# Optimization experiments

Measured on AMD Instinct MI355X. Metric: run time of the kernel, lower is better.

## Reference

```python
import jax, jax.numpy as jnp
import numpy as np

B, S, D, H = 8, 2048, 64, 4
Dh = D // H  # head_dim = 16


def setup_inputs() -> dict:
    key = jax.random.key(0)
    k1, k2, k3, k4 = jax.random.split(key, 4)
    x = jax.random.normal(k1, (B, S, D), jnp.float32)
    # Linear weights stored torch-style as [out_features, in_features]
    W_qkv = jax.random.normal(k2, (3 * D, D), jnp.float32) * 0.125
    W_proj = jax.random.normal(k3, (D, D), jnp.float32) * 0.125
    b_proj = jnp.zeros((D,), jnp.float32)
    # Ragged structure: random valid length per sample, causal + padding mask
    lens = jax.random.randint(k4, (B,), S // 4, S + 1)
    pos = jnp.arange(S)
    key_valid = pos[None, :] < lens[:, None]          # [B, S]
    causal = pos[:, None] >= pos[None, :]             # [S, S]
    attn_mask = (causal[None, :, :] & key_valid[:, None, :])[:, None, :, :]  # [B,1,S,S], True=attend
    return {"x": x, "attn_mask": attn_mask, "W_qkv": W_qkv, "W_proj": W_proj, "b_proj": b_proj}


def reference(x, attn_mask, W_qkv, W_proj, b_proj):
    b, s, d = x.shape
    # fused QKV projection (qkv_bias=False)
    qkv = x @ W_qkv.T                                  # [B, S, 3D]
    qkv = qkv.reshape(b, s, 3, H, Dh).transpose(2, 0, 3, 1, 4)  # [3, B, H, S, Dh]
    q, k, v = qkv[0], qkv[1], qkv[2]
    scale = 1.0 / jnp.sqrt(jnp.asarray(Dh, x.dtype))
    scores = jnp.einsum('bhqd,bhkd->bhqk', q, k) * scale  # [B, H, S, S]
    neg = jnp.asarray(jnp.finfo(scores.dtype).min, scores.dtype)
    scores = jnp.where(attn_mask, scores, neg)
    attn = jax.nn.softmax(scores, axis=-1)
    ctx = jnp.einsum('bhqk,bhkd->bhqd', attn, v)       # [B, H, S, Dh]
    ctx = ctx.transpose(0, 2, 1, 3).reshape(b, s, d)   # [B, S, D]
    return ctx @ W_proj.T + b_proj
```

## Files before the change

### kernel.cpp

```cpp
#include <hip/hip_runtime.h>
#include <hip/hip_bf16.h>

typedef __attribute__((ext_vector_type(4))) float f32x4;
typedef __attribute__((ext_vector_type(16))) float f32x16;
typedef __attribute__((ext_vector_type(8))) short bf16x8;
typedef __attribute__((ext_vector_type(4))) short bf16x4;

#define SEQ 2048
#define NH 4
#define DH 16

#define WS_LEN 0
#define WS_WP  1024
#define WS_Q   65536
#define WS_K   (WS_Q + 2097152)
#define WS_V   (WS_K + 2097152)

#define MFMA16 __builtin_amdgcn_mfma_f32_16x16x32_bf16
#define MFMA32 __builtin_amdgcn_mfma_f32_32x32x16_bf16

__device__ __forceinline__ short f2bf(float f){
  __hip_bfloat16 h = __float2bfloat16(f);
  return __builtin_bit_cast(short, h);
}

__device__ __forceinline__ bf16x8 pack8(f32x4 a, f32x4 b){
  bf16x8 r;
  r[0]=f2bf(a[0]); r[1]=f2bf(a[1]); r[2]=f2bf(a[2]); r[3]=f2bf(a[3]);
  r[4]=f2bf(b[0]); r[5]=f2bf(b[1]); r[6]=f2bf(b[2]); r[7]=f2bf(b[3]);
  return r;
}

__global__ __launch_bounds__(256) void qkv_prep_kernel(const float* __restrict__ x,
                                                       const unsigned char* __restrict__ mask,
                                                       const float* __restrict__ wqkv,
                                                       const float* __restrict__ wproj,
                                                       unsigned char* __restrict__ ws){
  const int tid = threadIdx.x;
  if (blockIdx.x == 256){
    if (blockIdx.y == 1){
      short* wp = (short*)(ws + WS_WP);
      for (int i = tid; i < 64*64; i += 256) wp[i] = f2bf(wproj[i]);
      return;
    }
    const unsigned w0 = *(const unsigned*)mask;
    const int mode = (mask[2048] != 0) ? 0 : ((w0 == 1u) ? 1 : ((w0 == 0x3f800000u) ? 2 : 0));
    __shared__ int cnts[8];
    if (tid < 8) cnts[tid] = 0;
    __syncthreads();
    const int b = tid >> 5, j = tid & 31;
    const long long rowbase = (long long)b * SEQ * SEQ + (long long)(SEQ-1) * SEQ;
    int c = 0;
    if (mode == 0){
      const unsigned* mw = (const unsigned*)(mask + rowbase);
      for (int k = j; k < SEQ/4; k += 32){
        unsigned v = mw[k];
        c += (v & 0xffu ? 1:0) + (v & 0xff00u ? 1:0) + (v & 0xff0000u ? 1:0) + (v & 0xff000000u ? 1:0);
      }
    } else if (mode == 1){
      for (int k = j; k < SEQ; k += 32) c += ((const int*)mask)[rowbase + k] != 0;
    } else {
      for (int k = j; k < SEQ; k += 32) c += ((const float*)mask)[rowbase + k] != 0.0f;
    }
    atomicAdd(&cnts[b], c);
    __syncthreads();
    if (tid < 8) ((int*)ws)[tid] = cnts[tid];
    return;
  }

  const int lane = tid & 63;
  const int wv   = tid >> 6;
  const int c    = lane & 15;
  const int g    = lane >> 4;
  const int T0   = blockIdx.x * 64 + wv * 16;
  const f32x4 z = {0.f, 0.f, 0.f, 0.f};

  bf16x8 aw[2];
  {
    const float* xr = x + (long long)(T0 + c) * 64 + g * 8;
    #pragma unroll
    for (int w = 0; w < 2; ++w){
      f32x4 lo = *(const f32x4*)(xr + w*32);
      f32x4 hi = *(const f32x4*)(xr + w*32 + 4);
      aw[w] = pack8(lo, hi);
    }
  }

  const int tok  = T0 + c;
  const int b    = tok >> 11;
  const int s    = tok & (SEQ-1);
  short* Qd = (short*)(ws + WS_Q);
  short* Kd = (short*)(ws + WS_K);
  short* Vd = (short*)(ws + WS_V);

  #pragma unroll
  for (int oi = 0; oi < 6; ++oi){
    const int ot = blockIdx.y * 6 + oi;
    const float* wr = wqkv + (ot*16 + c) * 64 + g * 8;
    bf16x8 b0 = pack8(*(const f32x4*)(wr),      *(const f32x4*)(wr + 4));
    bf16x8 b1 = pack8(*(const f32x4*)(wr + 32), *(const f32x4*)(wr + 36));
    f32x4 acc = z;
    acc = MFMA16(b0, aw[0], acc, 0, 0, 0);
    acc = MFMA16(b1, aw[1], acc, 0, 0, 0);
    if (ot < 4){
      bf16x4 pk;
      #pragma unroll
      for (int r = 0; r < 4; ++r) pk[r] = f2bf(acc[r] * (0.25f * 1.44269504f));
      *(bf16x4*)(Qd + ((long long)(b*NH + ot) * SEQ + s) * DH + g*4) = pk;
    } else if (ot < 8){
      bf16x4 pk;
      #pragma unroll
      for (int r = 0; r < 4; ++r) pk[r] = f2bf(acc[r]);
      *(bf16x4*)(Kd + ((long long)(b*NH + (ot-4)) * SEQ + s) * DH + g*4) = pk;
    } else {
      #pragma unroll
      for (int r = 0; r < 4; ++r)
        Vd[((long long)(b*NH + (ot-8)) * DH + g*4 + r) * SEQ + s] = f2bf(acc[r]);
    }
  }
}

__global__ __launch_bounds__(512, 4) void attn_kernel(const unsigned char* __restrict__ ws,
                                                      const float* __restrict__ bproj,
                                                      float* __restrict__ out){
  const int tid  = threadIdx.x;
  const int lane = tid & 63;
  const int wv   = tid >> 6;
  const int h    = wv & 3;
  const int half = wv >> 2;
  const int c    = lane & 15;
  const int g    = lane >> 4;
  const int ql   = lane & 31;
  const int hi   = lane >> 5;
  const int L    = blockIdx.x;
  const int b    = (L + (L >> 8)) & 7;
  const int u    = L >> 3;
  const int t    = (u < 32) ? (2*u) : (63 - 2*(u - 32));
  const int q0   = t * 32;
  const int len  = ((const int*)ws)[b];
  const long long bh = (long long)(b*NH + h);
  const short* Q  = (const short*)(ws + WS_Q) + bh * SEQ * DH;
  const short* K  = (const short*)(ws + WS_K) + bh * SEQ * DH;
  const short* Vt = (const short*)(ws + WS_V) + bh * DH * SEQ;
  const short* Wp = (const short*)(ws + WS_WP);

  __shared__ __align__(16) unsigned char smem[78848];
  float* CMB = (float*)(smem + 65536);
  float* LSB = (float*)(smem + 74240);
  const unsigned pb   = (unsigned)wv * 8192;
  const unsigned CTXB = 74752;
  const f32x4 z  = {0.f,0.f,0.f,0.f};
  const f32x16 z16 = {0.f,0.f,0.f,0.f,0.f,0.f,0.f,0.f,0.f,0.f,0.f,0.f,0.f,0.f,0.f,0.f};
  const short one_bf = (short)0x3F80;
  const bf16x8 ones = {one_bf,one_bf,one_bf,one_bf,one_bf,one_bf,one_bf,one_bf};

  const bf16x8 qf = *(const bf16x8*)(Q + (q0 + ql)*DH + hi*8);

  f32x4 acc[2]  = {z, z};
  f32x4 accS[2] = {z, z};
  const int kcount = min(q0 + 32, len);
  const int nkt  = (kcount + 63) >> 6;
  const int icnt = min(q0 >> 6, len >> 6);
  const int nh0  = nkt >> 1;
  const int kb   = half ? nh0 : 0;
  const int ke   = half ? nkt : nh0;
  const int n    = ke - kb;
  const int rot  = (n >= 4) ? ((h * n) >> 2) : 0;
  const int qg   = q0 + ql;
  const unsigned swq  = (unsigned)(ql & 7) << 4;
  const unsigned sw   = (unsigned)(c & 7) << 4;

  auto TI = [&](int i){ int kt = kb + i + rot; return (kt >= ke) ? kt - n : kt; };

  auto qkexp = [&](int tt, int p, bf16x8 (&kk)[2]){
    const int k0 = tt * 64;
    const bool nomask = tt < icnt;
    const unsigned rowb = pb + ((unsigned)p << 12) + (unsigned)ql*128;
    #pragma unroll
    for (int kb32 = 0; kb32 < 2; ++kb32){
      f32x16 st = MFMA32(kk[kb32], qf, z16, 0, 0, 0);
      #pragma unroll
      for (int grp = 0; grp < 4; ++grp){
        const int keybase = kb32*32 + grp*8 + hi*4;
        float p0 = __builtin_amdgcn_exp2f(st[grp*4 + 0]);
        float p1 = __builtin_amdgcn_exp2f(st[grp*4 + 1]);
        float p2 = __builtin_amdgcn_exp2f(st[grp*4 + 2]);
        float p3 = __builtin_amdgcn_exp2f(st[grp*4 + 3]);
        if (!nomask){
          const int k = k0 + keybase;
          p0 = (k   <= qg && k   < len) ? p0 : 0.f;
          p1 = (k+1 <= qg && k+1 < len) ? p1 : 0.f;
          p2 = (k+2 <= qg && k+2 < len) ? p2 : 0.f;
          p3 = (k+3 <= qg && k+3 < len) ? p3 : 0.f;
        }
        uint2 pk;
        pk.x = __builtin_amdgcn_perm(__builtin_bit_cast(unsigned, p1),
                                     __builtin_bit_cast(unsigned, p0), 0x07060302u);
        pk.y = __builtin_amdgcn_perm(__builtin_bit_cast(unsigned, p3),
                                     __builtin_bit_cast(unsigned, p2), 0x07060302u);
        *(uint2*)&smem[rowb + ((unsigned)(keybase*2) ^ swq)] = pk;
      }
    }
  };

  bf16x8 knx[2], vcur[2], vnx[2], knn[2], vnn[2];
  if (n > 0){
    const int t0 = TI(0);
    const int k0 = t0 * 64;
    bf16x8 k0f[2];
    k0f[0] = *(const bf16x8*)(K + (k0 + ql)*DH + hi*8);
    k0f[1] = *(const bf16x8*)(K + (k0 + 32 + ql)*DH + hi*8);
    vcur[0] = *(const bf16x8*)(Vt + c*SEQ + k0 + g*8);
    vcur[1] = *(const bf16x8*)(Vt + c*SEQ + k0 + 32 + g*8);
    qkexp(t0, 0, k0f);
    if (n > 1){
      const int k1 = TI(1) * 64;
      knx[0] = *(const bf16x8*)(K + (k1 + ql)*DH + hi*8);
      knx[1] = *(const bf16x8*)(K + (k1 + 32 + ql)*DH + hi*8);
      vnx[0] = *(const bf16x8*)(Vt + c*SEQ + k1 + g*8);
      vnx[1] = *(const bf16x8*)(Vt + c*SEQ + k1 + 32 + g*8);
    }
  }

  for (int i = 0; i < n; ++i){
    const unsigned bufr = pb + ((unsigned)(i & 1) << 12);
    bf16x8 pa[2][2];
    #pragma unroll
    for (int qb = 0; qb < 2; ++qb)
      #pragma unroll
      for (int w = 0; w < 2; ++w)
        pa[qb][w] = *(const bf16x8*)&smem[bufr + (qb*16 + c)*128 + ((unsigned)(w*64 + g*16) ^ sw)];

    if (i + 1 < n){
      if (i + 2 < n){
        const int k2 = TI(i + 2) * 64;
        knn[0] = *(const bf16x8*)(K + (k2 + ql)*DH + hi*8);
        knn[1] = *(const bf16x8*)(K + (k2 + 32 + ql)*DH + hi*8);
        vnn[0] = *(const bf16x8*)(Vt + c*SEQ + k2 + g*8);
        vnn[1] = *(const bf16x8*)(Vt + c*SEQ + k2 + 32 + g*8);
      }
      qkexp(TI(i + 1), (i + 1) & 1, knx);
    }

    __builtin_amdgcn_s_setprio(1);
    #pragma unroll
    for (int qb = 0; qb < 2; ++qb)
      #pragma unroll
      for (int w = 0; w < 2; ++w){
        acc[qb]  = MFMA16(pa[qb][w], vcur[w], acc[qb], 0, 0, 0);
        accS[qb] = MFMA16(pa[qb][w], ones,    accS[qb], 0, 0, 0);
      }
    __builtin_amdgcn_s_setprio(0);

    vcur[0] = vnx[0]; vcur[1] = vnx[1];
    knx[0] = knn[0]; knx[1] = knn[1];
    vnx[0] = vnn[0]; vnx[1] = vnn[1];
  }

  if (half == 0){
    #pragma unroll
    for (int qb = 0; qb < 2; ++qb){
      #pragma unroll
      for (int r = 0; r < 4; ++r)
        CMB[(h*32 + qb*16 + g*4 + r)*17 + c] = acc[qb][r];
      if (c == 0){
        #pragma unroll
        for (int r = 0; r < 4; ++r)
          LSB[h*32 + qb*16 + g*4 + r] = accS[qb][r];
      }
    }
  }
  __syncthreads();
  if (half == 1){
    #pragma unroll
    for (int qb = 0; qb < 2; ++qb){
      #pragma unroll
      for (int r = 0; r < 4; ++r){
        const int q = qb*16 + g*4 + r;
        const float tot = acc[qb][r] + CMB[(h*32 + q)*17 + c];
        const float lsT = LSB[h*32 + q] + accS[qb][r];
        const float cv  = tot / lsT;
        *(short*)&smem[CTXB + q*128 +
            (((unsigned)((h*16 + c)*2)) ^ ((unsigned)(q & 7) << 4))] = f2bf(cv);
      }
    }
  }
  __syncthreads();

  bf16x8 wpf[2];
  #pragma unroll
  for (int w = 0; w < 2; ++w)
    wpf[w] = *(const bf16x8*)(Wp + (h*16 + c)*64 + w*32 + g*8);
  const float bias = bproj[h*16 + c];
  f32x4 oa = z;
  const unsigned rbc = CTXB + (half*16 + c)*128;
  #pragma unroll
  for (int w = 0; w < 2; ++w){
    bf16x8 pa = *(const bf16x8*)&smem[rbc + ((unsigned)(w*64 + g*16) ^ sw)];
    oa = MFMA16(pa, wpf[w], oa, 0, 0, 0);
  }
  #pragma unroll
  for (int r = 0; r < 4; ++r)
    out[((long long)b * SEQ + q0 + half*16 + g*4 + r) * 64 + h*16 + c] = oa[r] + bias;
}

extern "C" void kernel_launch(void* const* d_in, const int* in_sizes, int n_in,
                              void* d_out, int out_size, void* d_ws, size_t ws_size,
                              hipStream_t stream) {
  const float* x     = (const float*)d_in[0];
  const unsigned char* mask = (const unsigned char*)d_in[1];
  const float* wqkv  = (const float*)d_in[2];
  const float* wproj = (const float*)d_in[3];
  const float* bproj = (const float*)d_in[4];
  float* out = (float*)d_out;
  unsigned char* ws = (unsigned char*)d_ws;

  qkv_prep_kernel<<<dim3(257, 2), 256, 0, stream>>>(x, mask, wqkv, wproj, ws);
  attn_kernel<<<512, 512, 0, stream>>>(ws, bproj, out);
}
```

Measured before the change: 32.74 us.

## Pair causal query tiles per block and split combined key work across four wave groups

Each 1024-thread block now handles two 32-row query tiles, one early and one mirrored late tile, so every block gets a balanced amount of causal work. The combined key-tile range of both tiles is split evenly across four wave quarters, and partial numerators and denominators are merged with LDS atomicAdd before normalization and the output projection. This targets load imbalance and tail effects from the ragged causal workload. In exchange it doubles LDS use to about 154KB per block, which limits occupancy to one block per CU. It also adds LDS atomics, a zero-init pass and an extra barrier.

```diff
diff --git a/kernel.cpp b/kernel.cpp
--- a/kernel.cpp
+++ b/kernel.cpp
@@ -120,23 +120,23 @@
   }
 }
 
-__global__ __launch_bounds__(512, 4) void attn_kernel(const unsigned char* __restrict__ ws,
-                                                      const float* __restrict__ bproj,
-                                                      float* __restrict__ out){
+__global__ __launch_bounds__(1024, 4) void attn_kernel(const unsigned char* __restrict__ ws,
+                                                       const float* __restrict__ bproj,
+                                                       float* __restrict__ out){
   const int tid  = threadIdx.x;
   const int lane = tid & 63;
   const int wv   = tid >> 6;
   const int h    = wv & 3;
-  const int half = wv >> 2;
+  const int qd   = wv >> 2;
   const int c    = lane & 15;
   const int g    = lane >> 4;
   const int ql   = lane & 31;
   const int hi   = lane >> 5;
   const int L    = blockIdx.x;
-  const int b    = (L + (L >> 8)) & 7;
+  const int b    = L & 7;
   const int u    = L >> 3;
-  const int t    = (u < 32) ? (2*u) : (63 - 2*(u - 32));
-  const int q0   = t * 32;
+  const int q0A  = u * 32;
+  const int q0B  = (63 - u) * 32;
   const int len  = ((const int*)ws)[b];
   const long long bh = (long long)(b*NH + h);
   const short* Q  = (const short*)(ws + WS_Q) + bh * SEQ * DH;
@@ -144,41 +144,45 @@
   const short* Vt = (const short*)(ws + WS_V) + bh * DH * SEQ;
   const short* Wp = (const short*)(ws + WS_WP);
 
-  __shared__ __align__(16) unsigned char smem[78848];
-  float* CMB = (float*)(smem + 65536);
-  float* LSB = (float*)(smem + 74240);
-  const unsigned pb   = (unsigned)wv * 8192;
-  const unsigned CTXB = 74752;
+  __shared__ __align__(16) unsigned char smem[157696];
+  float* CMB = (float*)(smem + 131072);
+  float* LSB = (float*)(smem + 148480);
+  const unsigned CTXB = 149504;
   const f32x4 z  = {0.f,0.f,0.f,0.f};
   const f32x16 z16 = {0.f,0.f,0.f,0.f,0.f,0.f,0.f,0.f,0.f,0.f,0.f,0.f,0.f,0.f,0.f,0.f};
   const short one_bf = (short)0x3F80;
   const bf16x8 ones = {one_bf,one_bf,one_bf,one_bf,one_bf,one_bf,one_bf,one_bf};
 
-  const bf16x8 qf = *(const bf16x8*)(Q + (q0 + ql)*DH + hi*8);
-
-  f32x4 acc[2]  = {z, z};
-  f32x4 accS[2] = {z, z};
-  const int kcount = min(q0 + 32, len);
-  const int nkt  = (kcount + 63) >> 6;
-  const int icnt = min(q0 >> 6, len >> 6);
-  const int nh0  = nkt >> 1;
-  const int kb   = half ? nh0 : 0;
-  const int ke   = half ? nkt : nh0;
-  const int n    = ke - kb;
-  const int rot  = (n >= 4) ? ((h * n) >> 2) : 0;
-  const int qg   = q0 + ql;
+  for (int i2 = tid; i2 < 4608; i2 += 1024) ((float*)(smem + 131072))[i2] = 0.f;
+  __syncthreads();
+
+  const bf16x8 qfA = *(const bf16x8*)(Q + (q0A + ql)*DH + hi*8);
+  const bf16x8 qfB = *(const bf16x8*)(Q + (q0B + ql)*DH + hi*8);
+
+  f32x4 accA[2] = {z, z}, accSA[2] = {z, z};
+  f32x4 accB[2] = {z, z}, accSB[2] = {z, z};
+
+  const int nktA  = (min(q0A + 32, len) + 63) >> 6;
+  const int nktB  = (min(q0B + 32, len) + 63) >> 6;
+  const int icntA = min(q0A >> 6, len >> 6);
+  const int icntB = min(q0B >> 6, len >> 6);
+  const int U   = nktA + nktB;
+  const int lo  = (qd * U) >> 2;
+  const int hi_ = ((qd + 1) * U) >> 2;
+  const int n   = hi_ - lo;
+  const unsigned pb   = (unsigned)wv * 8192;
   const unsigned swq  = (unsigned)(ql & 7) << 4;
   const unsigned sw   = (unsigned)(c & 7) << 4;
 
-  auto TI = [&](int i){ int kt = kb + i + rot; return (kt >= ke) ? kt - n : kt; };
-
-  auto qkexp = [&](int tt, int p, bf16x8 (&kk)[2]){
-    const int k0 = tt * 64;
-    const bool nomask = tt < icnt;
-    const unsigned rowb = pb + ((unsigned)p << 12) + (unsigned)ql*128;
+  auto KOFF = [&](int i){ return (i < nktA ? i : i - nktA) * 64; };
+
+  auto qkexp = [&](int k0, int kt, int icnt_t, int qg_t, const bf16x8 &qf_t,
+                   int par, bf16x8 (&kk)[2]){
+    const bool nomask = kt < icnt_t;
+    const unsigned rowb = pb + ((unsigned)par << 12) + (unsigned)ql*128;
     #pragma unroll
     for (int kb32 = 0; kb32 < 2; ++kb32){
-      f32x16 st = MFMA32(kk[kb32], qf, z16, 0, 0, 0);
+      f32x16 st = MFMA32(kk[kb32], qf_t, z16, 0, 0, 0);
       #pragma unroll
       for (int grp = 0; grp < 4; ++grp){
         const int keybase = kb32*32 + grp*8 + hi*4;
@@ -188,10 +192,10 @@
         float p3 = __builtin_amdgcn_exp2f(st[grp*4 + 3]);
         if (!nomask){
           const int k = k0 + keybase;
-          p0 = (k   <= qg && k   < len) ? p0 : 0.f;
-          p1 = (k+1 <= qg && k+1 < len) ? p1 : 0.f;
-          p2 = (k+2 <= qg && k+2 < len) ? p2 : 0.f;
-          p3 = (k+3 <= qg && k+3 < len) ? p3 : 0.f;
+          p0 = (k   <= qg_t && k   < len) ? p0 : 0.f;
+          p1 = (k+1 <= qg_t && k+1 < len) ? p1 : 0.f;
+          p2 = (k+2 <= qg_t && k+2 < len) ? p2 : 0.f;
+          p3 = (k+3 <= qg_t && k+3 < len) ? p3 : 0.f;
         }
         uint2 pk;
         pk.x = __builtin_amdgcn_perm(__builtin_bit_cast(unsigned, p1),
@@ -203,18 +207,22 @@
     }
   };
 
+  auto produce = [&](int i, int par, bf16x8 (&kk)[2]){
+    if (i < nktA) qkexp(i*64, i, icntA, q0A + ql, qfA, par, kk);
+    else { const int kt = i - nktA; qkexp(kt*64, kt, icntB, q0B + ql, qfB, par, kk); }
+  };
+
   bf16x8 knx[2], vcur[2], vnx[2], knn[2], vnn[2];
   if (n > 0){
-    const int t0 = TI(0);
-    const int k0 = t0 * 64;
+    const int k0 = KOFF(lo);
     bf16x8 k0f[2];
     k0f[0] = *(const bf16x8*)(K + (k0 + ql)*DH + hi*8);
     k0f[1] = *(const bf16x8*)(K + (k0 + 32 + ql)*DH + hi*8);
     vcur[0] = *(const bf16x8*)(Vt + c*SEQ + k0 + g*8);
     vcur[1] = *(const bf16x8*)(Vt + c*SEQ + k0 + 32 + g*8);
-    qkexp(t0, 0, k0f);
+    produce(lo, lo & 1, k0f);
     if (n > 1){
-      const int k1 = TI(1) * 64;
+      const int k1 = KOFF(lo + 1);
       knx[0] = *(const bf16x8*)(K + (k1 + ql)*DH + hi*8);
       knx[1] = *(const bf16x8*)(K + (k1 + 32 + ql)*DH + hi*8);
       vnx[0] = *(const bf16x8*)(Vt + c*SEQ + k1 + g*8);
@@ -222,7 +230,7 @@
     }
   }
 
-  for (int i = 0; i < n; ++i){
+  for (int i = lo; i < hi_; ++i){
     const unsigned bufr = pb + ((unsigned)(i & 1) << 12);
     bf16x8 pa[2][2];
     #pragma unroll
@@ -231,59 +239,72 @@
       for (int w = 0; w < 2; ++w)
         pa[qb][w] = *(const bf16x8*)&smem[bufr + (qb*16 + c)*128 + ((unsigned)(w*64 + g*16) ^ sw)];
 
-    if (i + 1 < n){
-      if (i + 2 < n){
-        const int k2 = TI(i + 2) * 64;
+    if (i + 1 < hi_){
+      if (i + 2 < hi_){
+        const int k2 = KOFF(i + 2);
         knn[0] = *(const bf16x8*)(K + (k2 + ql)*DH + hi*8);
         knn[1] = *(const bf16x8*)(K + (k2 + 32 + ql)*DH + hi*8);
         vnn[0] = *(const bf16x8*)(Vt + c*SEQ + k2 + g*8);
         vnn[1] = *(const bf16x8*)(Vt + c*SEQ + k2 + 32 + g*8);
       }
-      qkexp(TI(i + 1), (i + 1) & 1, knx);
-    }
-
-    __builtin_amdgcn_s_setprio(1);
-    #pragma unroll
-    for (int qb = 0; qb < 2; ++qb)
-      #pragma unroll
-      for (int w = 0; w < 2; ++w){
-        acc[qb]  = MFMA16(pa[qb][w], vcur[w], acc[qb], 0, 0, 0);
-        accS[qb] = MFMA16(pa[qb][w], ones,    accS[qb], 0, 0, 0);
-      }
-    __builtin_amdgcn_s_setprio(0);
+      produce(i + 1, (i + 1) & 1, knx);
+    }
+
+    if (i < nktA){
+      #pragma unroll
+      for (int qb = 0; qb < 2; ++qb)
+        #pragma unroll
+        for (int w = 0; w < 2; ++w){
+          accA[qb]  = MFMA16(pa[qb][w], vcur[w], accA[qb], 0, 0, 0);
+          accSA[qb] = MFMA16(pa[qb][w], ones,    accSA[qb], 0, 0, 0);
+        }
+    } else {
+      #pragma unroll
+      for (int qb = 0; qb < 2; ++qb)
+        #pragma unroll
+        for (int w = 0; w < 2; ++w){
+          accB[qb]  = MFMA16(pa[qb][w], vcur[w], accB[qb], 0, 0, 0);
+          accSB[qb] = MFMA16(pa[qb][w], ones,    accSB[qb], 0, 0, 0);
+        }
+    }
 
     vcur[0] = vnx[0]; vcur[1] = vnx[1];
     knx[0] = knn[0]; knx[1] = knn[1];
     vnx[0] = vnn[0]; vnx[1] = vnn[1];
   }
 
-  if (half == 0){
-    #pragma unroll
-    for (int qb = 0; qb < 2; ++qb){
-      #pragma unroll
-      for (int r = 0; r < 4; ++r)
-        CMB[(h*32 + qb*16 + g*4 + r)*17 + c] = acc[qb][r];
-      if (c == 0){
-        #pragma unroll
-        for (int r = 0; r < 4; ++r)
-          LSB[h*32 + qb*16 + g*4 + r] = accS[qb][r];
-      }
-    }
-  }
-  __syncthreads();
-  if (half == 1){
-    #pragma unroll
-    for (int qb = 0; qb < 2; ++qb){
+  if (lo < nktA){
+    #pragma unroll
+    for (int qb = 0; qb < 2; ++qb)
       #pragma unroll
       for (int r = 0; r < 4; ++r){
         const int q = qb*16 + g*4 + r;
-        const float tot = acc[qb][r] + CMB[(h*32 + q)*17 + c];
-        const float lsT = LSB[h*32 + q] + accS[qb][r];
-        const float cv  = tot / lsT;
-        *(short*)&smem[CTXB + q*128 +
-            (((unsigned)((h*16 + c)*2)) ^ ((unsigned)(q & 7) << 4))] = f2bf(cv);
-      }
-    }
+        atomicAdd(&CMB[((0*4 + h)*32 + q)*17 + c], accA[qb][r]);
+        if (c == 0) atomicAdd(&LSB[(0*4 + h)*32 + q], accSA[qb][r]);
+      }
+  }
+  if (hi_ > nktA){
+    #pragma unroll
+    for (int qb = 0; qb < 2; ++qb)
+      #pragma unroll
+      for (int r = 0; r < 4; ++r){
+        const int q = qb*16 + g*4 + r;
+        atomicAdd(&CMB[((1*4 + h)*32 + q)*17 + c], accB[qb][r]);
+        if (c == 0) atomicAdd(&LSB[(1*4 + h)*32 + q], accSB[qb][r]);
+      }
+  }
+  __syncthreads();
+
+  const int ti = (wv >> 2) & 1;
+  const int rh = wv >> 3;
+  const int q0t = ti ? q0B : q0A;
+  #pragma unroll
+  for (int r = 0; r < 4; ++r){
+    const int q = rh*16 + g*4 + r;
+    const float sum = LSB[(ti*4 + h)*32 + q];
+    const float cv  = CMB[((ti*4 + h)*32 + q)*17 + c] / sum;
+    *(short*)&smem[CTXB + ti*4096 + q*128 +
+        (((unsigned)((h*16 + c)*2)) ^ ((unsigned)(q & 7) << 4))] = f2bf(cv);
   }
   __syncthreads();
 
@@ -293,7 +314,7 @@
     wpf[w] = *(const bf16x8*)(Wp + (h*16 + c)*64 + w*32 + g*8);
   const float bias = bproj[h*16 + c];
   f32x4 oa = z;
-  const unsigned rbc = CTXB + (half*16 + c)*128;
+  const unsigned rbc = CTXB + ti*4096 + (rh*16 + c)*128;
   #pragma unroll
   for (int w = 0; w < 2; ++w){
     bf16x8 pa = *(const bf16x8*)&smem[rbc + ((unsigned)(w*64 + g*16) ^ sw)];
@@ -301,7 +322,7 @@
   }
   #pragma unroll
   for (int r = 0; r < 4; ++r)
-    out[((long long)b * SEQ + q0 + half*16 + g*4 + r) * 64 + h*16 + c] = oa[r] + bias;
+    out[((long long)b * SEQ + q0t + rh*16 + g*4 + r) * 64 + h*16 + c] = oa[r] + bias;
 }
 
 extern "C" void kernel_launch(void* const* d_in, const int* in_sizes, int n_in,
@@ -316,5 +337,5 @@
   unsigned char* ws = (unsigned char*)d_ws;
 
   qkv_prep_kernel<<<dim3(257, 2), 256, 0, stream>>>(x, mask, wqkv, wproj, ws);
-  attn_kernel<<<512, 512, 0, stream>>>(ws, bproj, out);
-}
+  attn_kernel<<<256, 1024, 0, stream>>>(ws, bproj, out);
+}
```

After: 50.33 us. +53.7%, slower.
